# Kernel optimization log

Measured on AMD Instinct MI355X. Metric: run time of the kernel, lower is better.

Reference implementation:

```python
import jax, jax.numpy as jnp
import numpy as np
from jax import lax

B, J, I = 32, 48, 48          # batch, target len, source len
W = 2                          # target_window_size
CTX = 2 * W + 1                # 5
E, H = 128, 256                # embedding_size, hidden_units
VT, VS = 32000, 32000          # target / source vocab
S = 2 * J                      # HMM states (word + null)


def setup_inputs() -> dict:
    key = jax.random.key(0)
    ks = jax.random.split(key, 12)
    inp = {
        "target_embedding": jax.random.normal(ks[0], (VT, E), jnp.float32) * 0.02,
        "W_bridge": jax.random.normal(ks[1], (E * CTX, E), jnp.float32) * 0.02,
        "W_hidden": jax.random.normal(ks[2], (E, H), jnp.float32) * 0.02,
        "b_hidden": jnp.zeros((H,), jnp.float32),
        "W_vocab": jax.random.normal(ks[3], (H, VS), jnp.float32) * 0.02,
        "b_vocab": jnp.zeros((VS,), jnp.float32),
        "transition": jax.random.uniform(ks[4], (B, S, S), jnp.float32, 0.01, 1.0),
        "initial_transition": jax.random.uniform(ks[5], (B, S), jnp.float32, 0.01, 1.0),
        "targets_ctx": jax.random.randint(ks[6], (B, J * CTX), 0, VT, jnp.int32),
        "targets_ctx_null": jax.random.randint(ks[7], (B, J * CTX), 0, VT, jnp.int32),
        "sources": jax.random.randint(ks[8], (B, I), 0, VS, jnp.int32),
    }
    return inp


def _emission(emb, Wb, Wh, bh, Wv, bv, ctx_ids, sources):
    # embedding lookup + context reshape: [B, J*CTX, E] -> [B, J, CTX*E]
    x = emb[ctx_ids].reshape(ctx_ids.shape[0], -1, CTX * E)
    h = jnp.tanh(jnp.einsum('bjc,ce,eh->bjh', x, Wb, Wh) + bh)  # bridge+hidden
    probs = jax.nn.softmax(h @ Wv + bv, axis=-1)                # [B, J, VS]
    # per-example gather of source token columns -> [B, J, I]
    return jax.vmap(lambda p, s: p[:, s])(probs, sources)


def _forward_backward(pi, A, em):
    # pi [B,S], A [B,S,S], em [B,S,I]; scaled HMM forward-backward
    e = jnp.moveaxis(em, 2, 0)  # [I, B, S]
    a0 = pi * e[0]
    c0 = a0.sum(-1, keepdims=True)
    a0 = a0 / c0

    def fstep(a, ei):
        an = jnp.einsum('bs,bst->bt', a, A) * ei
        c = an.sum(-1, keepdims=True)
        an = an / c
        return an, (an, c)

    _, (alphas, cs) = lax.scan(fstep, a0, e[1:])
    alphas = jnp.concatenate([a0[None], alphas], 0)          # [I,B,S]
    cs = jnp.concatenate([c0[None], cs], 0)                  # [I,B,1]

    def bstep(b, inp):
        ei, ci = inp
        bn = jnp.einsum('bst,bt->bs', A, ei * b) / ci
        return bn, bn

    bI = jnp.ones_like(a0)
    _, betas_rev = lax.scan(bstep, bI, (e[1:][::-1], cs[1:][::-1]))
    betas = jnp.concatenate([betas_rev[::-1], bI[None]], 0)  # [I,B,S]

    gamma = alphas * betas                                   # state posteriors
    loglik = jnp.log(cs[..., 0]).sum(0)                      # [B]
    return jnp.moveaxis(gamma, 0, 2), loglik


def reference(target_embedding, W_bridge, W_hidden, b_hidden, W_vocab, b_vocab,
              transition, initial_transition, targets_ctx, targets_ctx_null, sources):
    em_word = _emission(target_embedding, W_bridge, W_hidden, b_hidden,
                        W_vocab, b_vocab, targets_ctx, sources)       # [B,J,I]
    em_null = _emission(target_embedding, W_bridge, W_hidden, b_hidden,
                        W_vocab, b_vocab, targets_ctx_null, sources)  # [B,J,I]
    emission = jnp.concatenate([em_word, em_null], axis=1)            # [B,2J,I]
    gamma, loglik = _forward_backward(initial_transition, transition, emission)
    return gamma, -loglik
```

## Files before the change

### kernel.cpp

```cpp
#include <hip/hip_runtime.h>
#include <hip/hip_bf16.h>

#define NB 32
#define NJ 48
#define NI 48
#define NCTX 5
#define NE 128
#define NH 256
#define NVS 32000
#define NS 96
#define NR 3072

typedef __attribute__((ext_vector_type(8))) short bf16x8;
typedef __attribute__((ext_vector_type(4))) float f32x4;

__device__ __forceinline__ unsigned short f2b(float f) {
  __hip_bfloat16 h = __float2bfloat16(f);
  return *reinterpret_cast<unsigned short*>(&h);
}
__device__ __forceinline__ float wave_sum(float v) {
  v += __shfl_xor(v, 1);
  v += __shfl_xor(v, 2);
  v += __shfl_xor(v, 4);
  v += __shfl_xor(v, 8);
  v += __shfl_xor(v, 16);
  v += __shfl_xor(v, 32);
  return v;
}
__device__ __forceinline__ void gload_lds16(const void* g, void* l) {
  __builtin_amdgcn_global_load_lds(
      (const __attribute__((address_space(1))) void*)g,
      (__attribute__((address_space(3))) void*)l, 16, 0, 0);
}


__global__ __launch_bounds__(256) void k_transpose(const float* __restrict__ Wv,
                                                   unsigned char* __restrict__ Wv8) {
  __shared__ float tile[64][65];
  int t = threadIdx.x;
  int v0 = blockIdx.x * 64, k0 = blockIdx.y * 64;
  {
    int kr = t >> 4, vq = t & 15;
#pragma unroll
    for (int it = 0; it < 4; ++it) {
      float4 v = *(const float4*)&Wv[(k0 + kr + 16 * it) * NVS + v0 + vq * 4];
      tile[kr + 16 * it][vq * 4 + 0] = v.x;
      tile[kr + 16 * it][vq * 4 + 1] = v.y;
      tile[kr + 16 * it][vq * 4 + 2] = v.z;
      tile[kr + 16 * it][vq * 4 + 3] = v.w;
    }
  }
  __syncthreads();
  {
    int vl = t >> 2, kq = t & 3;
    unsigned int q8[4];
#pragma unroll
    for (int d = 0; d < 4; ++d) {
      float f0 = tile[kq * 16 + d * 4 + 0][vl] * 64.0f;
      float f1 = tile[kq * 16 + d * 4 + 1][vl] * 64.0f;
      float f2 = tile[kq * 16 + d * 4 + 2][vl] * 64.0f;
      float f3 = tile[kq * 16 + d * 4 + 3][vl] * 64.0f;
      int w = __builtin_amdgcn_cvt_pk_fp8_f32(f0, f1, 0, false);
      w = __builtin_amdgcn_cvt_pk_fp8_f32(f2, f3, w, true);
      q8[d] = (unsigned int)w;
    }
    int kqp = kq ^ ((vl >> 2) & 3);
    unsigned int q8s[4];
    if ((vl >> 1) & 1) {
      q8s[0] = q8[2]; q8s[1] = q8[3]; q8s[2] = q8[0]; q8s[3] = q8[1];
    } else {
      q8s[0] = q8[0]; q8s[1] = q8[1]; q8s[2] = q8[2]; q8s[3] = q8[3];
    }
    *(uint4*)&Wv8[(v0 + vl) * 256 + k0 + kqp * 16] = *(uint4*)q8s;
  }
}

__global__ __launch_bounds__(256) void k_t2b(const float* __restrict__ src,
                                             unsigned short* __restrict__ dst,
                                             int R, int C) {
  __shared__ float tile[64][65];
  int t = threadIdx.x;
  int r0 = blockIdx.x * 64, c0 = blockIdx.y * 64;
  {
    int rr = t >> 4, cq = t & 15;
#pragma unroll
    for (int it = 0; it < 4; ++it) {
      float4 v = *(const float4*)&src[(r0 + rr + 16 * it) * C + c0 + cq * 4];
      tile[rr + 16 * it][cq * 4 + 0] = v.x;
      tile[rr + 16 * it][cq * 4 + 1] = v.y;
      tile[rr + 16 * it][cq * 4 + 2] = v.z;
      tile[rr + 16 * it][cq * 4 + 3] = v.w;
    }
  }
  __syncthreads();
  {
    int cc = t >> 2, rq = t & 3;
    unsigned short pk[16];
#pragma unroll
    for (int q = 0; q < 16; ++q) pk[q] = f2b(tile[rq * 16 + q][cc]);
    *(uint4*)&dst[(c0 + cc) * R + r0 + rq * 16] = *(uint4*)&pk[0];
    *(uint4*)&dst[(c0 + cc) * R + r0 + rq * 16 + 8] = *(uint4*)&pk[8];
  }
}

__global__ __launch_bounds__(256) void k_xb(const float* __restrict__ emb,
                                            const unsigned short* __restrict__ Wbt,
                                            const int* __restrict__ tc, const int* __restrict__ tcn,
                                            unsigned short* __restrict__ xb) {
  __shared__ unsigned short Ax[32 * 72];
  __shared__ unsigned short Bw[128 * 72];
  __shared__ unsigned short xout[32 * 136];
  int t = threadIdx.x;
  int r0 = blockIdx.x * 32;
  int wave = t >> 6, lane = t & 63;
  int wm = wave >> 1, wn = wave & 1;
  int lg = lane >> 4, lr = lane & 15;
  int arow = t >> 3, aseg = t & 7;
  int r = r0 + arow;
  int half = r / 1536, rem = r % 1536, bb = rem / 48, jj = rem % 48;
  const int* ids = half ? tcn : tc;
  int brow = t >> 1, bseg = t & 1;

  f32x4 acc[4];
#pragma unroll
  for (int n = 0; n < 4; ++n) acc[n] = (f32x4){0.f, 0.f, 0.f, 0.f};

  for (int step = 0; step < 10; ++step) {
    int k0 = step * 64;
    int p = step >> 1;
    int e0 = (step & 1) * 64;
    {
      int id = ids[bb * 240 + jj * 5 + p];
      const float4* er = (const float4*)&emb[id * 128 + e0 + aseg * 8];
      float4 v0 = er[0], v1 = er[1];
      unsigned short pk[8];
      pk[0] = f2b(v0.x); pk[1] = f2b(v0.y); pk[2] = f2b(v0.z); pk[3] = f2b(v0.w);
      pk[4] = f2b(v1.x); pk[5] = f2b(v1.y); pk[6] = f2b(v1.z); pk[7] = f2b(v1.w);
      *(uint4*)&Ax[arow * 72 + aseg * 8] = *(uint4*)&pk[0];
    }
    {
      const uint4* wp = (const uint4*)&Wbt[brow * 640 + k0 + bseg * 32];
      uint4* dp = (uint4*)&Bw[brow * 72 + bseg * 32];
      uint4 w0 = wp[0], w1 = wp[1], w2 = wp[2], w3 = wp[3];
      dp[0] = w0; dp[1] = w1; dp[2] = w2; dp[3] = w3;
    }
    __syncthreads();
#pragma unroll
    for (int kk = 0; kk < 2; ++kk) {
      bf16x8 a = *(const bf16x8*)&Ax[(wm * 16 + lr) * 72 + kk * 32 + lg * 8];
#pragma unroll
      for (int n = 0; n < 4; ++n) {
        bf16x8 b = *(const bf16x8*)&Bw[(wn * 64 + n * 16 + lr) * 72 + kk * 32 + lg * 8];
        acc[n] = __builtin_amdgcn_mfma_f32_16x16x32_bf16(a, b, acc[n], 0, 0, 0);
      }
    }
    __syncthreads();
  }
#pragma unroll
  for (int n = 0; n < 4; ++n)
#pragma unroll
    for (int g = 0; g < 4; ++g)
      xout[(wm * 16 + lg * 4 + g) * 136 + wn * 64 + n * 16 + lr] = f2b(acc[n][g]);
  __syncthreads();
  {
    int orow = t >> 3, os = t & 7;
    *(uint4*)&xb[(r0 + orow) * 128 + os * 16] = *(uint4*)&xout[orow * 136 + os * 16];
    *(uint4*)&xb[(r0 + orow) * 128 + os * 16 + 8] = *(uint4*)&xout[orow * 136 + os * 16 + 8];
  }
}

__global__ __launch_bounds__(256) void k_h(const unsigned short* __restrict__ xb,
                                           const unsigned short* __restrict__ Wht,
                                           const float* __restrict__ bh,
                                           unsigned char* __restrict__ hb8) {
  __shared__ char smem[69632];
  unsigned short* Asm = (unsigned short*)smem;
  unsigned short* Bsm = (unsigned short*)(smem + 34816);
  unsigned char* o8 = (unsigned char*)smem;
  int t = threadIdx.x;
  int r0 = blockIdx.x * 128, n0 = blockIdx.y * 128;
  int wave = t >> 6, lane = t & 63;
  int wm = wave >> 1, wn = wave & 1;
  int lg = lane >> 4, lr = lane & 15;
  {
    int row = t >> 1, seg = t & 1;
#pragma unroll
    for (int i = 0; i < 8; ++i) {
      *(uint4*)&Asm[row * 136 + seg * 64 + i * 8] = *(const uint4*)&xb[(r0 + row) * 128 + seg * 64 + i * 8];
      *(uint4*)&Bsm[row * 136 + seg * 64 + i * 8] = *(const uint4*)&Wht[(n0 + row) * 128 + seg * 64 + i * 8];
    }
  }
  __syncthreads();
  f32x4 acc[4][4];
#pragma unroll
  for (int m = 0; m < 4; ++m)
#pragma unroll
    for (int n = 0; n < 4; ++n) acc[m][n] = (f32x4){0.f, 0.f, 0.f, 0.f};
#pragma unroll
  for (int kk = 0; kk < 4; ++kk) {
    bf16x8 a[4], b[4];
#pragma unroll
    for (int m = 0; m < 4; ++m)
      a[m] = *(const bf16x8*)&Asm[(wm * 64 + m * 16 + lr) * 136 + kk * 32 + lg * 8];
#pragma unroll
    for (int n = 0; n < 4; ++n)
      b[n] = *(const bf16x8*)&Bsm[(wn * 64 + n * 16 + lr) * 136 + kk * 32 + lg * 8];
#pragma unroll
    for (int m = 0; m < 4; ++m)
#pragma unroll
      for (int n = 0; n < 4; ++n)
        acc[m][n] = __builtin_amdgcn_mfma_f32_16x16x32_bf16(a[m], b[n], acc[m][n], 0, 0, 0);
  }
  __syncthreads();
#pragma unroll
  for (int n = 0; n < 4; ++n) {
    int cl = wn * 64 + n * 16 + lr;
    float bvv = bh[n0 + cl];
#pragma unroll
    for (int m = 0; m < 4; ++m) {
#pragma unroll
      for (int g = 0; g < 4; ++g) {
        int rl = wm * 64 + m * 16 + lg * 4 + g;
        float hv = tanhf(acc[m][n][g] + bvv);
        int p8 = __builtin_amdgcn_cvt_pk_fp8_f32(hv * 256.0f, 0.0f, 0, false);
        o8[rl * 144 + cl] = (unsigned char)(p8 & 0xFF);
      }
    }
  }
  __syncthreads();
  {
    int row = t >> 1, seg = t & 1;
    int sig = (row >> 1) & 7;
    int swp = row & 1;
#pragma unroll
    for (int i = 0; i < 4; ++i) {
      int p_loc = seg * 4 + i;
      int w_loc = p_loc ^ sig;
      unsigned long long q[2];
      q[0] = *(const unsigned long long*)&o8[row * 144 + w_loc * 16 + swp * 8];
      q[1] = *(const unsigned long long*)&o8[row * 144 + w_loc * 16 + (swp ^ 1) * 8];
      *(uint4*)&hb8[(r0 + row) * 256 + n0 + p_loc * 16] = *(uint4*)q;
    }
  }
}

__global__ __launch_bounds__(256) void k_denom(const unsigned char* __restrict__ hb8,
                                               const unsigned char* __restrict__ Wv8,
                                               const float* __restrict__ bv,
                                               float* __restrict__ dpart) {
  __shared__ __align__(16) unsigned char Asm[32768];
  int t = threadIdx.x;
  int bid = blockIdx.x;
  int xcd = bid & 7;
  int pos = bid >> 3;
  int tile = xcd * 375 + pos;
  int vtp = tile / 24, rt = tile % 24;
  int r0 = rt * 128;
  int wave = t >> 6, lane = t & 63;
  int wm = wave >> 1, wn = wave & 1;
  int lg = lane >> 4, lr = lane & 15;

#pragma unroll
  for (int c = 0; c < 8; ++c) {
    int inst = wave * 8 + c;
    gload_lds16(&hb8[(r0 + inst * 4 + (lane >> 4)) * 256 + (lane & 15) * 16], &Asm[inst * 1024]);
  }
  __syncthreads();

  long long a_reg[4][8];
#pragma unroll
  for (int m = 0; m < 4; ++m) {
    int rowb = (wm * 64 + m * 16 + lr) * 256;
#pragma unroll
    for (int s = 0; s < 8; ++s)
      a_reg[m][s] = *(const long long*)&Asm[rowb + (((s * 4 + lg) ^ lr) << 3)];
  }

  const float SC = 6.103515625e-05f;
  int sg = (lr >> 1) & 7;

#pragma unroll
  for (int vt = 0; vt < 2; ++vt) {
    const unsigned char* Bp = Wv8 + ((size_t)((vtp * 2 + vt) * 128 + wn * 64 + lr)) * 256;
    f32x4 acc[4][4];
#pragma unroll
    for (int m = 0; m < 4; ++m)
#pragma unroll
      for (int n = 0; n < 4; ++n) acc[m][n] = (f32x4){0.f, 0.f, 0.f, 0.f};

#pragma unroll
    for (int ks = 0; ks < 4; ++ks) {
#pragma unroll
      for (int kk = 0; kk < 2; ++kk) {
        int so = ks * 64 + ((((kk << 2) + lg) ^ sg) << 3);
        long long b[4];
#pragma unroll
        for (int n = 0; n < 4; ++n)
          b[n] = *(const long long*)(Bp + n * 4096 + so);
        __builtin_amdgcn_s_setprio(1);
#pragma unroll
        for (int m = 0; m < 4; ++m)
#pragma unroll
          for (int n = 0; n < 4; ++n)
            acc[m][n] = __builtin_amdgcn_mfma_f32_16x16x32_fp8_fp8(a_reg[m][ks * 2 + kk], b[n],
                                                                   acc[m][n], 0, 0, 0);
        __builtin_amdgcn_s_setprio(0);
      }
    }
    int v0 = (vtp * 2 + vt) * 128;
    float rs[4][4];
#pragma unroll
    for (int m = 0; m < 4; ++m)
#pragma unroll
      for (int g = 0; g < 4; ++g) rs[m][g] = 0.f;
#pragma unroll
    for (int m = 0; m < 4; ++m) {
#pragma unroll
      for (int n = 0; n < 4; ++n) {
        float bvv = bv[v0 + wn * 64 + n * 16 + lr];
#pragma unroll
        for (int g = 0; g < 4; ++g) rs[m][g] += __expf(acc[m][n][g] * SC + bvv);
      }
    }
#pragma unroll
    for (int m = 0; m < 4; ++m)
#pragma unroll
      for (int g = 0; g < 4; ++g) {
        float v = rs[m][g];
        v += __shfl_xor(v, 1);
        v += __shfl_xor(v, 2);
        v += __shfl_xor(v, 4);
        v += __shfl_xor(v, 8);
        rs[m][g] = v;
      }
    if (lr == 0) {
      int d = (vtp * 2 + vt) * 2 + wn;
#pragma unroll
      for (int m = 0; m < 4; ++m)
#pragma unroll
        for (int g = 0; g < 4; ++g)
          dpart[d * NR + r0 + wm * 64 + m * 16 + lg * 4 + g] = rs[m][g];
    }
  }
}

__global__ void k_reduce(const float* __restrict__ dpart, float* __restrict__ dsum) {
  int r = blockIdx.x * 256 + threadIdx.x;
  float s = 0.f;
  for (int vt = 0; vt < 500; ++vt) s += dpart[vt * NR + r];
  dsum[r] = s;
}

__global__ __launch_bounds__(64) void k_emis(const unsigned char* __restrict__ hb8,
                                             const unsigned char* __restrict__ Wv8,
                                             const float* __restrict__ bv,
                                             const float* __restrict__ dsum,
                                             const int* __restrict__ src,
                                             float* __restrict__ em) {
  __shared__ unsigned char A8[48 * 256];
  __shared__ unsigned char B8[48 * 256];
  __shared__ int s_src[48];
  int t = threadIdx.x;
  int bh = blockIdx.x;
  int b = bh & 31, half = bh >> 5;
  int row4 = t >> 4, seg = t & 15;
  int rbase = half * 1536 + b * 48;
  if (t < 48) s_src[t] = src[b * 48 + t];
#pragma unroll
  for (int c = 0; c < 12; ++c) {
    int row = c * 4 + row4;
    gload_lds16(&hb8[(rbase + row) * 256 + seg * 16], &A8[c * 1024]);
    int sv = src[b * 48 + row];
    gload_lds16(&Wv8[sv * 256 + seg * 16], &B8[c * 1024]);
  }
  __syncthreads();
  int lg = t >> 4, lr = t & 15;
  int svr[3];
#pragma unroll
  for (int m = 0; m < 3; ++m) svr[m] = s_src[m * 16 + lr];
  f32x4 acc[3][3];
#pragma unroll
  for (int m = 0; m < 3; ++m)
#pragma unroll
    for (int n = 0; n < 3; ++n) acc[m][n] = (f32x4){0.f, 0.f, 0.f, 0.f};
#pragma unroll
  for (int kk = 0; kk < 8; ++kk) {
    int sa = kk * 4 + lg;
    long long a[3], bb[3];
#pragma unroll
    for (int m = 0; m < 3; ++m) {
      int rr = m * 16 + lr;
      a[m] = *(const long long*)&A8[rr * 256 + ((sa ^ lr) << 3)];
      bb[m] = *(const long long*)&B8[rr * 256 + ((sa >> 3) << 6) +
                                     (((sa & 7) ^ ((svr[m] >> 1) & 7)) << 3)];
    }
#pragma unroll
    for (int m = 0; m < 3; ++m)
#pragma unroll
      for (int n = 0; n < 3; ++n)
        acc[m][n] = __builtin_amdgcn_mfma_f32_16x16x32_fp8_fp8(a[m], bb[n], acc[m][n], 0, 0, 0);
  }
  const float SC = 6.103515625e-05f;
#pragma unroll
  for (int n = 0; n < 3; ++n) {
    int i = n * 16 + lr;
    float bvv = bv[svr[n]];
#pragma unroll
    for (int m = 0; m < 3; ++m) {
#pragma unroll
      for (int g = 0; g < 4; ++g) {
        int j = m * 16 + lg * 4 + g;
        float val = __expf(acc[m][n][g] * SC + bvv) / dsum[rbase + j];
        em[b * 4608 + (half * 48 + j) * 48 + i] = val;
      }
    }
  }
}

__global__ __launch_bounds__(192) void k_fb(const float* __restrict__ Atr, const float* __restrict__ pi,
                                            const float* __restrict__ em, float* __restrict__ alph,
                                            float* __restrict__ betas, float* __restrict__ out1) {
  __shared__ float A_st[96 * 97];
  __shared__ float em_lds[48 * 97];
  __shared__ __align__(16) float vec_lds[96];
  __shared__ float red[3];
  int t = threadIdx.x;
  int bid = blockIdx.x;
  int b = bid & 31;
  int role = bid >> 5;
  int col = t >> 1, half = t & 1;
  int base = b * 4608;

  for (int idx = t; idx < 96 * 96; idx += 192) {
    int s = idx / 96, tt = idx % 96;
    A_st[s * 97 + tt] = Atr[b * 9216 + idx];
  }
  for (int idx = t; idx < 96 * 48; idx += 192) {
    int s = idx / 48, i = idx % 48;
    em_lds[i * 97 + s] = em[base + idx];
  }
  __syncthreads();

  float Areg[48];
  if (role == 0) {
#pragma unroll
    for (int ss = 0; ss < 48; ++ss) Areg[ss] = A_st[(half * 48 + ss) * 97 + col];

    float llsum;
    {
      float v = pi[b * 96 + col] * em_lds[0 * 97 + col];
      float ws = half ? 0.f : v;
      ws = wave_sum(ws);
      if ((t & 63) == 0) red[t >> 6] = ws;
      __syncthreads();
      float c = red[0] + red[1] + red[2];
      float a = v / c;
      if (!half) {
        vec_lds[col] = a;
        alph[base + col] = a;
      }
      llsum = logf(c);
      __syncthreads();
    }
    for (int i = 1; i < 48; ++i) {
      float p = 0.f;
      const float4* ap = (const float4*)&vec_lds[half * 48];
#pragma unroll
      for (int q = 0; q < 12; ++q) {
        float4 av = ap[q];
        p += av.x * Areg[4 * q] + av.y * Areg[4 * q + 1] + av.z * Areg[4 * q + 2] + av.w * Areg[4 * q + 3];
      }
      p += __shfl_xor(p, 1);
      float an = p * em_lds[i * 97 + col];
      float ws = half ? 0.f : an;
      ws = wave_sum(ws);
      if ((t & 63) == 0) red[t >> 6] = ws;
      __syncthreads();
      float c = red[0] + red[1] + red[2];
      float a = an / c;
      if (!half) {
        vec_lds[col] = a;
        alph[base + i * 96 + col] = a;
      }
      llsum += logf(c);
      __syncthreads();
    }
    if (t == 0) out1[b] = -llsum;
  } else {
#pragma unroll
    for (int tt = 0; tt < 48; ++tt) Areg[tt] = A_st[col * 97 + half * 48 + tt];

    if (!half) {
      betas[base + 47 * 96 + col] = 1.0f;
      vec_lds[col] = em_lds[47 * 97 + col];
    }
    __syncthreads();
    for (int i = 46; i >= 0; --i) {
      float p = 0.f;
      const float4* ep = (const float4*)&vec_lds[half * 48];
#pragma unroll
      for (int q = 0; q < 12; ++q) {
        float4 ev = ep[q];
        p += ev.x * Areg[4 * q] + ev.y * Areg[4 * q + 1] + ev.z * Areg[4 * q + 2] + ev.w * Areg[4 * q + 3];
      }
      p += __shfl_xor(p, 1);
      float ws = half ? 0.f : p;
      ws = wave_sum(ws);
      if ((t & 63) == 0) red[t >> 6] = ws;
      __syncthreads();
      float c = red[0] + red[1] + red[2];
      float bt = p / c;
      if (!half) {
        betas[base + i * 96 + col] = bt;
        vec_lds[col] = em_lds[i * 97 + col] * bt;
      }
      __syncthreads();
    }
  }
}

__global__ __launch_bounds__(128) void k_gamma(const float* __restrict__ alph,
                                               const float* __restrict__ betas,
                                               float* __restrict__ out0) {
  __shared__ float red[2];
  int b = blockIdx.x, i = blockIdx.y;
  int t = threadIdx.x;
  float g = 0.f;
  if (t < 96) g = alph[b * 4608 + i * 96 + t] * betas[b * 4608 + i * 96 + t];
  float ws = wave_sum(g);
  if ((t & 63) == 0) red[t >> 6] = ws;
  __syncthreads();
  float c = red[0] + red[1];
  if (t < 96) out0[b * 4608 + t * 48 + i] = g / c;
}

extern "C" void kernel_launch(void* const* d_in, const int* in_sizes, int n_in,
                              void* d_out, int out_size, void* d_ws, size_t ws_size,
                              hipStream_t stream) {
  const float* emb = (const float*)d_in[0];
  const float* Wb  = (const float*)d_in[1];
  const float* Wh  = (const float*)d_in[2];
  const float* bh  = (const float*)d_in[3];
  const float* Wv  = (const float*)d_in[4];
  const float* bv  = (const float*)d_in[5];
  const float* Atr = (const float*)d_in[6];
  const float* pi  = (const float*)d_in[7];
  const int* tc    = (const int*)d_in[8];
  const int* tcn   = (const int*)d_in[9];
  const int* src   = (const int*)d_in[10];

  float* out0 = (float*)d_out;
  float* out1 = out0 + NB * NS * NI;

  char* ws = (char*)d_ws;
  unsigned char* wv8 = (unsigned char*)(ws);
  unsigned char* hb8 = (unsigned char*)(ws + 8192000);
  float* dpart       = (float*)(ws + 8978432);
  float* betas       = (float*)(ws + 8978432);
  float* dsum        = (float*)(ws + 15122432);
  float* em          = (float*)(ws + 15134720);
  float* alph        = (float*)(ws + 15724544);
  unsigned short* wbt = (unsigned short*)(ws + 16314368);
  unsigned short* wht = (unsigned short*)(ws + 16478208);
  unsigned short* xb  = (unsigned short*)(ws + 16543744);

  k_transpose<<<dim3(500, 4), 256, 0, stream>>>(Wv, wv8);
  k_t2b<<<dim3(10, 2), 256, 0, stream>>>(Wb, wbt, 640, 128);
  k_t2b<<<dim3(2, 4), 256, 0, stream>>>(Wh, wht, 128, 256);
  k_xb<<<96, 256, 0, stream>>>(emb, wbt, tc, tcn, xb);
  k_h<<<dim3(24, 2), 256, 0, stream>>>(xb, wht, bh, hb8);
  k_denom<<<3000, 256, 0, stream>>>(hb8, wv8, bv, dpart);
  k_reduce<<<12, 256, 0, stream>>>(dpart, dsum);
  k_emis<<<64, 64, 0, stream>>>(hb8, wv8, bv, dsum, src, em);
  k_fb<<<64, 192, 0, stream>>>(Atr, pi, em, alph, betas, out1);
  k_gamma<<<dim3(32, 48), 128, 0, stream>>>(alph, betas, out0);
}
```

Measured before the change: 168.8 us.

## Stage W_vocab tiles through LDS with a 4-buffer async prefetch pipeline in k_denom

The denominator GEMM kernel no longer reads B (W_vocab fp8) fragments directly from global memory inside the MFMA loop. It streams 8 k-slices through four LDS buffers using direct global-to-LDS loads, prefetching two slices ahead with vmcnt-based waits and barriers. The bias loads are also hoisted to the kernel start, and the row sums are written out once at the end. This is meant to hide global-load latency behind the MFMAs, at the cost of more LDS (48KB), which may reduce occupancy, and extra barriers.

Result: faster. 161.8 us (-4.1%).

```diff
diff --git a/kernel.cpp b/kernel.cpp
--- a/kernel.cpp
+++ b/kernel.cpp
@@ -248,7 +248,8 @@
                                                const unsigned char* __restrict__ Wv8,
                                                const float* __restrict__ bv,
                                                float* __restrict__ dpart) {
-  __shared__ __align__(16) unsigned char Asm[32768];
+  __shared__ __align__(16) unsigned char smem[49152];
+  unsigned char* Asm = smem;
   int t = threadIdx.x;
   int bid = blockIdx.x;
   int xcd = bid & 7;
@@ -260,12 +261,31 @@
   int wm = wave >> 1, wn = wave & 1;
   int lg = lane >> 4, lr = lane & 15;
 
+  unsigned char* bufs[4] = {smem + 32768, smem + 40960, smem + 0, smem + 8192};
+
+  float bvv[2][4];
+#pragma unroll
+  for (int vt = 0; vt < 2; ++vt)
+#pragma unroll
+    for (int n = 0; n < 4; ++n)
+      bvv[vt][n] = bv[(vtp * 2 + vt) * 128 + wn * 64 + n * 16 + lr];
+  asm volatile("s_waitcnt vmcnt(0)" ::: "memory");
+
 #pragma unroll
   for (int c = 0; c < 8; ++c) {
     int inst = wave * 8 + c;
     gload_lds16(&hb8[(r0 + inst * 4 + (lane >> 4)) * 256 + (lane & 15) * 16], &Asm[inst * 1024]);
   }
-  __syncthreads();
+#pragma unroll
+  for (int s = 0; s < 2; ++s) {
+#pragma unroll
+    for (int c = 0; c < 2; ++c) {
+      int i = wave * 2 + c;
+      gload_lds16(&Wv8[((size_t)(vtp * 256 + i * 16 + (lane >> 2))) * 256 + s * 64 + (lane & 3) * 16],
+                  bufs[s] + i * 1024);
+    }
+  }
+  asm volatile("s_waitcnt vmcnt(4)\n\ts_barrier" ::: "memory");
 
   long long a_reg[4][8];
 #pragma unroll
@@ -275,71 +295,95 @@
     for (int s = 0; s < 8; ++s)
       a_reg[m][s] = *(const long long*)&Asm[rowb + (((s * 4 + lg) ^ lr) << 3)];
   }
+  asm volatile("s_waitcnt lgkmcnt(0)\n\ts_barrier" ::: "memory");
 
   const float SC = 6.103515625e-05f;
-  int sg = (lr >> 1) & 7;
-
-#pragma unroll
-  for (int vt = 0; vt < 2; ++vt) {
-    const unsigned char* Bp = Wv8 + ((size_t)((vtp * 2 + vt) * 128 + wn * 64 + lr)) * 256;
-    f32x4 acc[4][4];
-#pragma unroll
-    for (int m = 0; m < 4; ++m)
-#pragma unroll
-      for (int n = 0; n < 4; ++n) acc[m][n] = (f32x4){0.f, 0.f, 0.f, 0.f};
-
-#pragma unroll
-    for (int ks = 0; ks < 4; ++ks) {
-#pragma unroll
-      for (int kk = 0; kk < 2; ++kk) {
-        int so = ks * 64 + ((((kk << 2) + lg) ^ sg) << 3);
-        long long b[4];
+  f32x4 acc[4][4];
+#pragma unroll
+  for (int m = 0; m < 4; ++m)
+#pragma unroll
+    for (int n = 0; n < 4; ++n) acc[m][n] = (f32x4){0.f, 0.f, 0.f, 0.f};
+  float rs_all[2][4][4];
+
+#pragma unroll
+  for (int s = 0; s < 8; ++s) {
+    if (s < 6) {
+      int ns = s + 2;
+      int nvt = ns >> 2, nks = ns & 3;
+      size_t vb2 = (size_t)((vtp * 2 + nvt) * 128);
+#pragma unroll
+      for (int c = 0; c < 2; ++c) {
+        int i = wave * 2 + c;
+        gload_lds16(&Wv8[(vb2 + i * 16 + (lane >> 2)) * 256 + nks * 64 + (lane & 3) * 16],
+                    bufs[ns & 3] + i * 1024);
+      }
+    }
+    if (s < 6)
+      asm volatile("s_waitcnt vmcnt(4)\n\ts_barrier" ::: "memory");
+    else if (s == 6)
+      asm volatile("s_waitcnt vmcnt(2)\n\ts_barrier" ::: "memory");
+    else
+      asm volatile("s_waitcnt vmcnt(0)\n\ts_barrier" ::: "memory");
+
+    int ks = s & 3;
+    const unsigned char* bp = bufs[s & 3];
+#pragma unroll
+    for (int kk = 0; kk < 2; ++kk) {
+      long long b[4];
+#pragma unroll
+      for (int n = 0; n < 4; ++n) {
+        int rr = wn * 64 + n * 16 + lr;
+        b[n] = *(const long long*)&bp[rr * 64 + ((((kk << 2) + lg) ^ ((lr >> 1) & 7)) << 3)];
+      }
+      __builtin_amdgcn_s_setprio(1);
+#pragma unroll
+      for (int m = 0; m < 4; ++m)
 #pragma unroll
         for (int n = 0; n < 4; ++n)
-          b[n] = *(const long long*)(Bp + n * 4096 + so);
-        __builtin_amdgcn_s_setprio(1);
-#pragma unroll
-        for (int m = 0; m < 4; ++m)
-#pragma unroll
-          for (int n = 0; n < 4; ++n)
-            acc[m][n] = __builtin_amdgcn_mfma_f32_16x16x32_fp8_fp8(a_reg[m][ks * 2 + kk], b[n],
-                                                                   acc[m][n], 0, 0, 0);
-        __builtin_amdgcn_s_setprio(0);
-      }
-    }
-    int v0 = (vtp * 2 + vt) * 128;
-    float rs[4][4];
-#pragma unroll
-    for (int m = 0; m < 4; ++m)
-#pragma unroll
-      for (int g = 0; g < 4; ++g) rs[m][g] = 0.f;
-#pragma unroll
-    for (int m = 0; m < 4; ++m) {
-#pragma unroll
-      for (int n = 0; n < 4; ++n) {
-        float bvv = bv[v0 + wn * 64 + n * 16 + lr];
-#pragma unroll
-        for (int g = 0; g < 4; ++g) rs[m][g] += __expf(acc[m][n][g] * SC + bvv);
-      }
-    }
-#pragma unroll
-    for (int m = 0; m < 4; ++m)
-#pragma unroll
-      for (int g = 0; g < 4; ++g) {
-        float v = rs[m][g];
-        v += __shfl_xor(v, 1);
-        v += __shfl_xor(v, 2);
-        v += __shfl_xor(v, 4);
-        v += __shfl_xor(v, 8);
-        rs[m][g] = v;
-      }
-    if (lr == 0) {
+          acc[m][n] = __builtin_amdgcn_mfma_f32_16x16x32_fp8_fp8(a_reg[m][ks * 2 + kk], b[n],
+                                                                 acc[m][n], 0, 0, 0);
+      __builtin_amdgcn_s_setprio(0);
+    }
+    if (ks == 3) {
+      int vt = s >> 2;
+      float rs[4][4];
+#pragma unroll
+      for (int m = 0; m < 4; ++m)
+#pragma unroll
+        for (int g = 0; g < 4; ++g) rs[m][g] = 0.f;
+#pragma unroll
+      for (int m = 0; m < 4; ++m) {
+#pragma unroll
+        for (int n = 0; n < 4; ++n) {
+          float bvvv = bvv[vt][n];
+#pragma unroll
+          for (int g = 0; g < 4; ++g) rs[m][g] += __expf(acc[m][n][g] * SC + bvvv);
+          acc[m][n] = (f32x4){0.f, 0.f, 0.f, 0.f};
+        }
+      }
+#pragma unroll
+      for (int m = 0; m < 4; ++m)
+#pragma unroll
+        for (int g = 0; g < 4; ++g) {
+          float v = rs[m][g];
+          v += __shfl_xor(v, 1);
+          v += __shfl_xor(v, 2);
+          v += __shfl_xor(v, 4);
+          v += __shfl_xor(v, 8);
+          rs_all[vt][m][g] = v;
+        }
+    }
+  }
+
+  if (lr == 0) {
+#pragma unroll
+    for (int vt = 0; vt < 2; ++vt) {
       int d = (vtp * 2 + vt) * 2 + wn;
 #pragma unroll
       for (int m = 0; m < 4; ++m)
 #pragma unroll
         for (int g = 0; g < 4; ++g)
-          dpart[d * NR + r0 + wm * 64 + m * 16 + lg * 4 + g] = rs[m][g];
+          dpart[(size_t)d * NR + r0 + wm * 64 + m * 16 + lg * 4 + g] = rs_all[vt][m][g];
     }
   }
 }
```

## Use scaled 16x16x128 FP8 MFMA with LDS double-buffered B tiles in denominator kernel

Applied to the files above, without the earlier changes.

The denominator GEMM switches from 16x16x32 FP8 MFMAs, which read B directly from global memory, to the MI355X scaled 16x16x128 f8f6f4 MFMA. The scale operands fold the fixed dequantisation factor into the instruction, so the per-element multiply in the epilogue goes away. B tiles are staged through LDS with a double-buffered, swizzled global-to-LDS prefetch, and the A fragments are repacked into 256-bit operands. The cross-tile reduction kernel is also re-parallelised, with 16 lanes per row and a shuffle reduction, to use more blocks. This adds extra barriers per stage, and correctness depends on the exponent-scale encoding matching the old constant.

Result: faster. 147.3 us (-12.8%).

```diff
diff --git a/kernel.cpp b/kernel.cpp
--- a/kernel.cpp
+++ b/kernel.cpp
@@ -13,6 +13,7 @@
 
 typedef __attribute__((ext_vector_type(8))) short bf16x8;
 typedef __attribute__((ext_vector_type(4))) float f32x4;
+typedef __attribute__((ext_vector_type(8))) int i32x8;
 
 __device__ __forceinline__ unsigned short f2b(float f) {
   __hip_bfloat16 h = __float2bfloat16(f);
@@ -248,13 +249,12 @@
                                                const unsigned char* __restrict__ Wv8,
                                                const float* __restrict__ bv,
                                                float* __restrict__ dpart) {
-  __shared__ __align__(16) unsigned char Asm[32768];
+  __shared__ __align__(16) unsigned char smem[32768];
   int t = threadIdx.x;
   int bid = blockIdx.x;
-  int xcd = bid & 7;
-  int pos = bid >> 3;
-  int tile = xcd * 375 + pos;
-  int vtp = tile / 24, rt = tile % 24;
+  int xcd = bid & 7, pos = bid >> 3;
+  int tl = xcd * 375 + pos;
+  int vtp = tl / 24, rt = tl % 24;
   int r0 = rt * 128;
   int wave = t >> 6, lane = t & 63;
   int wm = wave >> 1, wn = wave & 1;
@@ -263,92 +263,138 @@
 #pragma unroll
   for (int c = 0; c < 8; ++c) {
     int inst = wave * 8 + c;
-    gload_lds16(&hb8[(r0 + inst * 4 + (lane >> 4)) * 256 + (lane & 15) * 16], &Asm[inst * 1024]);
-  }
-  __syncthreads();
-
-  long long a_reg[4][8];
+    gload_lds16(&hb8[(size_t)(r0 + inst * 4 + (lane >> 4)) * 256 + (lane & 15) * 16],
+                &smem[inst * 1024]);
+  }
+  __syncthreads();
+  i32x8 a_frag[4][2];
 #pragma unroll
   for (int m = 0; m < 4; ++m) {
     int rowb = (wm * 64 + m * 16 + lr) * 256;
 #pragma unroll
-    for (int s = 0; s < 8; ++s)
-      a_reg[m][s] = *(const long long*)&Asm[rowb + (((s * 4 + lg) ^ lr) << 3)];
-  }
-
-  const float SC = 6.103515625e-05f;
-  int sg = (lr >> 1) & 7;
-
-#pragma unroll
-  for (int vt = 0; vt < 2; ++vt) {
-    const unsigned char* Bp = Wv8 + ((size_t)((vtp * 2 + vt) * 128 + wn * 64 + lr)) * 256;
-    f32x4 acc[4][4];
+    for (int k = 0; k < 2; ++k) {
+      union { long long l[4]; i32x8 v; } u;
+#pragma unroll
+      for (int j = 0; j < 4; ++j)
+        u.l[j] = *(const long long*)&smem[rowb + (((k * 16 + lg * 4 + j) ^ lr) << 3)];
+      a_frag[m][k] = u.v;
+    }
+  }
+  __syncthreads();
+
+#pragma unroll
+  for (int c = 0; c < 4; ++c) {
+    int inst = wave * 4 + c;
+    gload_lds16(&Wv8[(size_t)(vtp * 256 + inst * 8 + (lane >> 3)) * 256 + (lane & 7) * 16],
+                &smem[inst * 1024]);
+  }
+  __syncthreads();
+
+  const unsigned int sa = 0x71717171u;
+  const unsigned int sb = 0x7F7F7F7Fu;
+  f32x4 acc[4][4];
+#pragma unroll
+  for (int m = 0; m < 4; ++m)
+#pragma unroll
+    for (int n = 0; n < 4; ++n) acc[m][n] = (f32x4){0.f, 0.f, 0.f, 0.f};
+  float rs_all[2][4][4];
+
+#pragma unroll
+  for (int s = 0; s < 4; ++s) {
+    if (s < 3) {
+      int ns = s + 1;
+      int nvt = ns >> 1, nk = ns & 1;
+#pragma unroll
+      for (int c = 0; c < 4; ++c) {
+        int inst = wave * 4 + c;
+        gload_lds16(&Wv8[(size_t)((vtp * 2 + nvt) * 128 + inst * 8 + (lane >> 3)) * 256 +
+                         nk * 128 + (lane & 7) * 16],
+                    &smem[((ns & 1) << 14) + inst * 1024]);
+      }
+    }
+    const unsigned char* bp = &smem[(s & 1) << 14];
+    i32x8 bfr[4];
+#pragma unroll
+    for (int n = 0; n < 4; ++n) {
+      int rr = wn * 64 + n * 16 + lr;
+      int sig = (rr >> 1) & 7;
+      union { long long l[4]; i32x8 v; } u;
+#pragma unroll
+      for (int j = 0; j < 4; ++j) {
+        int lb = lg * 32 + j * 8;
+        int h = lb >> 6;
+        int sl = (lb >> 3) & 7;
+        u.l[j] = *(const long long*)&bp[rr * 128 + h * 64 + ((sl ^ sig) << 3)];
+      }
+      bfr[n] = u.v;
+    }
+    int k = s & 1;
+    __builtin_amdgcn_s_setprio(1);
 #pragma unroll
     for (int m = 0; m < 4; ++m)
 #pragma unroll
-      for (int n = 0; n < 4; ++n) acc[m][n] = (f32x4){0.f, 0.f, 0.f, 0.f};
-
-#pragma unroll
-    for (int ks = 0; ks < 4; ++ks) {
-#pragma unroll
-      for (int kk = 0; kk < 2; ++kk) {
-        int so = ks * 64 + ((((kk << 2) + lg) ^ sg) << 3);
-        long long b[4];
-#pragma unroll
-        for (int n = 0; n < 4; ++n)
-          b[n] = *(const long long*)(Bp + n * 4096 + so);
-        __builtin_amdgcn_s_setprio(1);
-#pragma unroll
-        for (int m = 0; m < 4; ++m)
-#pragma unroll
-          for (int n = 0; n < 4; ++n)
-            acc[m][n] = __builtin_amdgcn_mfma_f32_16x16x32_fp8_fp8(a_reg[m][ks * 2 + kk], b[n],
-                                                                   acc[m][n], 0, 0, 0);
-        __builtin_amdgcn_s_setprio(0);
-      }
-    }
-    int v0 = (vtp * 2 + vt) * 128;
-    float rs[4][4];
-#pragma unroll
-    for (int m = 0; m < 4; ++m)
-#pragma unroll
-      for (int g = 0; g < 4; ++g) rs[m][g] = 0.f;
-#pragma unroll
-    for (int m = 0; m < 4; ++m) {
-#pragma unroll
-      for (int n = 0; n < 4; ++n) {
-        float bvv = bv[v0 + wn * 64 + n * 16 + lr];
-#pragma unroll
-        for (int g = 0; g < 4; ++g) rs[m][g] += __expf(acc[m][n][g] * SC + bvv);
-      }
-    }
-#pragma unroll
-    for (int m = 0; m < 4; ++m)
-#pragma unroll
-      for (int g = 0; g < 4; ++g) {
-        float v = rs[m][g];
-        v += __shfl_xor(v, 1);
-        v += __shfl_xor(v, 2);
-        v += __shfl_xor(v, 4);
-        v += __shfl_xor(v, 8);
-        rs[m][g] = v;
-      }
-    if (lr == 0) {
+      for (int n = 0; n < 4; ++n)
+        acc[m][n] = __builtin_amdgcn_mfma_scale_f32_16x16x128_f8f6f4(
+            a_frag[m][k], bfr[n], acc[m][n], 0, 0, 0, sa, 0, sb);
+    __builtin_amdgcn_s_setprio(0);
+    if (k == 1) {
+      int vt = s >> 1;
+      int v0 = (vtp * 2 + vt) * 128;
+      float rs[4][4];
+#pragma unroll
+      for (int m = 0; m < 4; ++m)
+#pragma unroll
+        for (int g = 0; g < 4; ++g) rs[m][g] = 0.f;
+#pragma unroll
+      for (int m = 0; m < 4; ++m) {
+#pragma unroll
+        for (int n = 0; n < 4; ++n) {
+          float bvv = bv[v0 + wn * 64 + n * 16 + lr];
+#pragma unroll
+          for (int g = 0; g < 4; ++g) rs[m][g] += __expf(acc[m][n][g] + bvv);
+          acc[m][n] = (f32x4){0.f, 0.f, 0.f, 0.f};
+        }
+      }
+#pragma unroll
+      for (int m = 0; m < 4; ++m)
+#pragma unroll
+        for (int g = 0; g < 4; ++g) {
+          float v = rs[m][g];
+          v += __shfl_xor(v, 1);
+          v += __shfl_xor(v, 2);
+          v += __shfl_xor(v, 4);
+          v += __shfl_xor(v, 8);
+          rs_all[vt][m][g] = v;
+        }
+    }
+    __syncthreads();
+  }
+
+  if (lr == 0) {
+#pragma unroll
+    for (int vt = 0; vt < 2; ++vt) {
       int d = (vtp * 2 + vt) * 2 + wn;
 #pragma unroll
       for (int m = 0; m < 4; ++m)
 #pragma unroll
         for (int g = 0; g < 4; ++g)
-          dpart[d * NR + r0 + wm * 64 + m * 16 + lg * 4 + g] = rs[m][g];
-    }
-  }
-}
-
-__global__ void k_reduce(const float* __restrict__ dpart, float* __restrict__ dsum) {
-  int r = blockIdx.x * 256 + threadIdx.x;
+          dpart[(size_t)d * NR + r0 + wm * 64 + m * 16 + lg * 4 + g] = rs_all[vt][m][g];
+    }
+  }
+}
+
+__global__ __launch_bounds__(256) void k_reduce(const float* __restrict__ dpart,
+                                                float* __restrict__ dsum) {
+  int t = threadIdx.x;
+  int r = blockIdx.x * 16 + (t >> 4);
+  int q = t & 15;
   float s = 0.f;
-  for (int vt = 0; vt < 500; ++vt) s += dpart[vt * NR + r];
-  dsum[r] = s;
+  for (int vt = q; vt < 500; vt += 16) s += dpart[(size_t)vt * NR + r];
+  s += __shfl_xor(s, 1);
+  s += __shfl_xor(s, 2);
+  s += __shfl_xor(s, 4);
+  s += __shfl_xor(s, 8);
+  if (q == 0) dsum[r] = s;
 }
 
 __global__ __launch_bounds__(64) void k_emis(const unsigned char* __restrict__ hb8,
@@ -570,7 +616,7 @@
   k_xb<<<96, 256, 0, stream>>>(emb, wbt, tc, tcn, xb);
   k_h<<<dim3(24, 2), 256, 0, stream>>>(xb, wht, bh, hb8);
   k_denom<<<3000, 256, 0, stream>>>(hb8, wv8, bv, dpart);
-  k_reduce<<<12, 256, 0, stream>>>(dpart, dsum);
+  k_reduce<<<192, 256, 0, stream>>>(dpart, dsum);
   k_emis<<<64, 64, 0, stream>>>(hb8, wv8, bv, dsum, src, em);
   k_fb<<<64, 192, 0, stream>>>(Atr, pi, em, alph, betas, out1);
   k_gamma<<<dim3(32, 48), 128, 0, stream>>>(alph, betas, out0);
```
